# Optimization experiments

Measured on AMD Instinct MI355X. Metric: run time of the kernel, lower is better.

Reference implementation:

```python
import jax, jax.numpy as jnp
import numpy as np

SIGMA = 0.1

def setup_inputs() -> dict:
    key = jax.random.key(0)
    k1, k2, k3 = jax.random.split(key, 3)
    B, BANDS, P, K = 128, 256, 32, 64
    x = jax.random.normal(k1, (B, 1, BANDS, P, P), dtype=jnp.float32)
    mu = 0.001 * jax.random.normal(k2, (BANDS,), dtype=jnp.float32)
    noise = jax.random.normal(k3, (BANDS,), dtype=jnp.float32)
    extra_noise = jnp.zeros((BANDS,), dtype=jnp.float32)
    return {"x": x, "mu": mu, "noise": noise, "extra_noise": extra_noise, "k": K}


def reference(x, mu, noise, extra_noise, k):
    # stochastic gate: z = mu + sigma*(noise + 0.25*extra_noise) (training=True, discount=1)
    z = mu + SIGMA * (noise + 0.25 * extra_noise)
    gate = jnp.clip(z + 0.5, 0.0, 1.0)  # hard_sigmoid, [bands]

    xs = x[:, 0]  # squeeze -> [B, bands, P, P]
    # stable top-k: with no ties this equals sorted top-k indices
    _, idx = jax.lax.top_k(gate, k)
    idx = jnp.sort(idx)  # [k]

    xg = xs[:, idx]  # gather bands -> [B, k, P, P]
    # transpose(1,3) * gate[topk] * transpose(1,3) == broadcast over band axis
    out = xg * gate[idx][None, :, None, None]
    return out[:, None]  # unsqueeze(1) -> [B, 1, k, P, P]
```

## Files before the change

### kernel.cpp

```cpp
#include <hip/hip_runtime.h>

#define SIGMA 0.1f
#define BANDS 256
#define KSEL  64
#define GTHREADS 512
#define PPB      8

typedef float vfloat4 __attribute__((ext_vector_type(4)));

__global__ void FeatureSelector_topk(const float* __restrict__ mu,
                                     const float* __restrict__ noise,
                                     const float* __restrict__ extra,
                                     int*   __restrict__ ws_idx,
                                     float* __restrict__ ws_gate) {
    __shared__ float g[BANDS];
    __shared__ unsigned long long masks[BANDS / 64];
    const int tid  = threadIdx.x;
    const int wave = tid >> 6;
    const int lane = tid & 63;

    float z = mu[tid] + SIGMA * (noise[tid] + 0.25f * extra[tid]) + 0.5f;
    float gate = fminf(fmaxf(z, 0.0f), 1.0f);
    g[tid] = gate;
    __syncthreads();

    int rank = 0;
#pragma unroll 16
    for (int j = 0; j < BANDS; ++j) {
        float gj = g[j];
        rank += (gj > gate) || (gj == gate && j < tid);
    }
    const bool sel = rank < KSEL;

    unsigned long long m = __ballot(sel);
    if (lane == 0) masks[wave] = m;
    __syncthreads();

    if (sel) {
        int pos = __popcll(m & ((1ull << lane) - 1ull));
        for (int w = 0; w < wave; ++w) pos += __popcll(masks[w]);
        ws_idx[pos]  = tid;
        ws_gate[pos] = gate;
    }
}

__global__ void __launch_bounds__(GTHREADS)
FeatureSelector_gather(const vfloat4* __restrict__ x,
                       const int*     __restrict__ ws_idx,
                       const float*   __restrict__ ws_gate,
                       vfloat4*       __restrict__ out) {
    const int bj0 = blockIdx.x * PPB;
    const int b   = bj0 >> 6;
    const int j0  = bj0 & (KSEL - 1);
    const int tid = threadIdx.x;
    const int jt  = tid >> 8;
    const int t   = tid & 255;

    constexpr int STEPS = PPB / 2;

    int   band[STEPS];
    float s[STEPS];
#pragma unroll
    for (int p = 0; p < STEPS; ++p) {
        band[p] = ws_idx[j0 + 2 * p + jt];
        s[p]    = ws_gate[j0 + 2 * p + jt];
    }

    vfloat4 v[STEPS];
#pragma unroll
    for (int p = 0; p < STEPS; ++p)
        v[p] = __builtin_nontemporal_load(&x[(b * BANDS + band[p]) * 256 + t]);
#pragma unroll
    for (int p = 0; p < STEPS; ++p) {
        v[p] *= s[p];
        __builtin_nontemporal_store(v[p], &out[(b * KSEL + j0 + 2 * p + jt) * 256 + t]);
    }
}

extern "C" void kernel_launch(void* const* d_in, const int* in_sizes, int n_in,
                              void* d_out, int out_size, void* d_ws, size_t ws_size,
                              hipStream_t stream) {
    const float* x     = (const float*)d_in[0];
    const float* mu    = (const float*)d_in[1];
    const float* noise = (const float*)d_in[2];
    const float* extra = (const float*)d_in[3];

    int*   ws_idx  = (int*)d_ws;
    float* ws_gate = (float*)((char*)d_ws + KSEL * sizeof(int));

    FeatureSelector_topk<<<1, BANDS, 0, stream>>>(mu, noise, extra, ws_idx, ws_gate);

    const int B = 128;
    FeatureSelector_gather<<<(B * KSEL) / PPB, GTHREADS, 0, stream>>>(
        (const vfloat4*)x, ws_idx, ws_gate, (vfloat4*)d_out);
}
```

Baseline: 192.6 us.

## Fuse top-k gate selection into gather kernel, recomputing per block

Merges the single-block top-k kernel into the gather kernel, so every block recomputes the gates, ranks them and compacts the selected indices into shared memory before gathering. This removes one kernel launch, the inter-kernel dependency and the workspace round trip. In exchange, each block repeats a 256-step ranking loop and adds block-wide barriers before its memory traffic starts.

```diff
diff --git a/kernel.cpp b/kernel.cpp
--- a/kernel.cpp
+++ b/kernel.cpp
@@ -8,51 +8,56 @@
 
 typedef float vfloat4 __attribute__((ext_vector_type(4)));
 
-__global__ void FeatureSelector_topk(const float* __restrict__ mu,
-                                     const float* __restrict__ noise,
-                                     const float* __restrict__ extra,
-                                     int*   __restrict__ ws_idx,
-                                     float* __restrict__ ws_gate) {
+__global__ void __launch_bounds__(GTHREADS)
+FeatureSelector_fused(const float*   __restrict__ mu,
+                      const float*   __restrict__ noise,
+                      const float*   __restrict__ extra,
+                      const vfloat4* __restrict__ x,
+                      vfloat4*       __restrict__ out) {
     __shared__ float g[BANDS];
     __shared__ unsigned long long masks[BANDS / 64];
-    const int tid  = threadIdx.x;
-    const int wave = tid >> 6;
-    const int lane = tid & 63;
+    __shared__ int   sidx[KSEL];
+    __shared__ float sgate[KSEL];
 
-    float z = mu[tid] + SIGMA * (noise[tid] + 0.25f * extra[tid]) + 0.5f;
-    float gate = fminf(fmaxf(z, 0.0f), 1.0f);
-    g[tid] = gate;
+    const int tid = threadIdx.x;
+
+    float gate = 0.0f;
+    bool  sel  = false;
+    unsigned long long m = 0;
+
+    if (tid < BANDS) {
+        float z = mu[tid] + SIGMA * (noise[tid] + 0.25f * extra[tid]) + 0.5f;
+        gate = fminf(fmaxf(z, 0.0f), 1.0f);
+        g[tid] = gate;
+    }
     __syncthreads();
 
-    int rank = 0;
+    if (tid < BANDS) {
+        int rank = 0;
 #pragma unroll 16
-    for (int j = 0; j < BANDS; ++j) {
-        float gj = g[j];
-        rank += (gj > gate) || (gj == gate && j < tid);
+        for (int j = 0; j < BANDS; ++j) {
+            float gj = g[j];
+            rank += (gj > gate) || (gj == gate && j < tid);
+        }
+        sel = rank < KSEL;
+        m = __ballot(sel);
+        if ((tid & 63) == 0) masks[tid >> 6] = m;
     }
-    const bool sel = rank < KSEL;
-
-    unsigned long long m = __ballot(sel);
-    if (lane == 0) masks[wave] = m;
     __syncthreads();
 
     if (sel) {
+        const int lane = tid & 63;
+        const int wave = tid >> 6;
         int pos = __popcll(m & ((1ull << lane) - 1ull));
         for (int w = 0; w < wave; ++w) pos += __popcll(masks[w]);
-        ws_idx[pos]  = tid;
-        ws_gate[pos] = gate;
+        sidx[pos]  = tid;
+        sgate[pos] = gate;
     }
-}
+    __syncthreads();
 
-__global__ void __launch_bounds__(GTHREADS)
-FeatureSelector_gather(const vfloat4* __restrict__ x,
-                       const int*     __restrict__ ws_idx,
-                       const float*   __restrict__ ws_gate,
-                       vfloat4*       __restrict__ out) {
     const int bj0 = blockIdx.x * PPB;
     const int b   = bj0 >> 6;
     const int j0  = bj0 & (KSEL - 1);
-    const int tid = threadIdx.x;
     const int jt  = tid >> 8;
     const int t   = tid & 255;
 
@@ -62,8 +67,8 @@
     float s[STEPS];
 #pragma unroll
     for (int p = 0; p < STEPS; ++p) {
-        band[p] = ws_idx[j0 + 2 * p + jt];
-        s[p]    = ws_gate[j0 + 2 * p + jt];
+        band[p] = sidx[j0 + 2 * p + jt];
+        s[p]    = sgate[j0 + 2 * p + jt];
     }
 
     vfloat4 v[STEPS];
@@ -85,12 +90,7 @@
     const float* noise = (const float*)d_in[2];
     const float* extra = (const float*)d_in[3];
 
-    int*   ws_idx  = (int*)d_ws;
-    float* ws_gate = (float*)((char*)d_ws + KSEL * sizeof(int));
-
-    FeatureSelector_topk<<<1, BANDS, 0, stream>>>(mu, noise, extra, ws_idx, ws_gate);
-
     const int B = 128;
-    FeatureSelector_gather<<<(B * KSEL) / PPB, GTHREADS, 0, stream>>>(
-        (const vfloat4*)x, ws_idx, ws_gate, (vfloat4*)d_out);
+    FeatureSelector_fused<<<(B * KSEL) / PPB, GTHREADS, 0, stream>>>(
+        mu, noise, extra, (const vfloat4*)x, (vfloat4*)d_out);
 }
```

New measurement: 197.5 us. 2.5% more time.
